# Kernel tuning notes

Measured on AMD Instinct MI355X. Metric: run time of the kernel, lower is better.

Reference implementation:

```python
import jax, jax.numpy as jnp
import numpy as np
import math

N = 50000      # nodes
E = 800000     # edges (avg degree 16)
T = 4          # time steps
F = 64         # feature dim (in = hidden = out)
MAX_LEN = 200  # positional encoding table length
EPS = 1e-5     # BatchNorm eps


def _make_pe(time_dim, max_len):
    pe = np.zeros((max_len, time_dim), dtype=np.float32)
    position = np.arange(max_len, dtype=np.float32)[:, None]
    div_term = np.exp(np.arange(0, time_dim, 2, dtype=np.float32) * (-math.log(10000.0) / time_dim))
    pe[:, 0::2] = np.sin(position * div_term)
    pe[:, 1::2] = np.cos(position * div_term)
    return jnp.asarray(pe)


def setup_inputs() -> dict:
    key = jax.random.key(0)
    ks = jax.random.split(key, 10)
    xav = math.sqrt(2.0 / (F + F))  # xavier_normal_ std for square linear
    return {
        "node_features": jax.random.normal(ks[0], (N, T, F), dtype=jnp.float32),
        "edges_weight": jax.random.uniform(ks[1], (T, E), dtype=jnp.float32),
        "identities": jax.random.randint(ks[2], (T,), 0, MAX_LEN),
        "edge_src": jax.random.randint(ks[3], (E,), 0, N),
        "edge_dst": jax.random.randint(ks[4], (E,), 0, N),
        "pe": _make_pe(F, MAX_LEN),
        "W0": jax.random.normal(ks[5], (F, F), dtype=jnp.float32) * xav,
        "W1": jax.random.normal(ks[6], (F, F), dtype=jnp.float32) * xav,
        "g0": jnp.ones((F,), jnp.float32),
        "b0": jnp.zeros((F,), jnp.float32),
        "g1": jnp.ones((F,), jnp.float32),
        "b1": jnp.zeros((F,), jnp.float32),
    }


def _gcn_layer(h, ew, edge_src, edge_dst, W):
    # gather-mul-scatter: msg_e = h[src_e] * w_e ; agg_v = sum_{e: dst=v} msg_e
    msg = h[edge_src] * ew                                   # (E, T, F)
    agg = jax.ops.segment_sum(msg, edge_dst, num_segments=N)  # (N, T, F)
    readout = agg.mean(axis=0)                                # dgl.mean_nodes (single graph) -> (T, F)
    return agg @ W, readout @ W


def _batchnorm(x, gamma, beta):
    # training-mode batch stats over all non-channel dims
    mean = x.mean(axis=(0, 1))
    var = x.var(axis=(0, 1))
    return (x - mean) * jax.lax.rsqrt(var + EPS) * gamma + beta


def reference(node_features, edges_weight, identities, edge_src, edge_dst,
              pe, W0, W1, g0, b0, g1, b1):
    # positional encoding added per time step
    h = node_features + pe[identities]          # (N, T, F)
    ew = edges_weight.T[:, :, None]             # (E, T, 1)
    # layer 0: gcn -> dropout(eval=identity) -> BN -> ReLU
    h, readout = _gcn_layer(h, ew, edge_src, edge_dst, W0)
    h = jax.nn.relu(_batchnorm(h, g0, b0))
    # layer 1 (output layer)
    h, readout = _gcn_layer(h, ew, edge_src, edge_dst, W1)
    h = jax.nn.relu(_batchnorm(h, g1, b1))
    return h, readout
```

## Files before the change

### kernel.cpp

```cpp
#include <hip/hip_runtime.h>

#define TF 256

typedef __attribute__((ext_vector_type(8))) short short8;
typedef __attribute__((ext_vector_type(4))) float f32x4;
typedef __attribute__((ext_vector_type(4))) unsigned int uint4v;
typedef __attribute__((ext_vector_type(2))) unsigned int uint2v;

__device__ inline unsigned short f2bf(float x) {
  unsigned u = __float_as_uint(x);
  u += 0x7fffu + ((u >> 16) & 1u);
  return (unsigned short)(u >> 16);
}
__device__ inline unsigned pack2(unsigned short lo, unsigned short hi) {
  return (unsigned)lo | ((unsigned)hi << 16);
}
__device__ inline float bflo(unsigned u) { return __uint_as_float(u << 16); }
__device__ inline float bfhi(unsigned u) { return __uint_as_float(u & 0xffff0000u); }

__global__ void prep_hist_kernel(const float* __restrict__ x, const float* __restrict__ pe,
                                 const int* __restrict__ ids, uint2v* __restrict__ h0, int n4,
                                 const int* __restrict__ dst, int* __restrict__ indeg, int E) {
  const int gid = blockIdx.x * blockDim.x + threadIdx.x;
  const int stride = gridDim.x * blockDim.x;
  for (int i = gid; i < n4; i += stride) {
    int e0 = (i << 2) & (TF - 1);
    int t = e0 >> 6;
    int f4 = e0 & 63;
    f32x4 v = __builtin_nontemporal_load(&reinterpret_cast<const f32x4*>(x)[i]);
    const f32x4 p = *reinterpret_cast<const f32x4*>(&pe[ids[t] * 64 + f4]);
    uint2v o;
    o.x = pack2(f2bf(v.x + p.x), f2bf(v.y + p.y));
    o.y = pack2(f2bf(v.z + p.z), f2bf(v.w + p.w));
    h0[i] = o;
  }
  for (int e = gid; e < E; e += stride) {
    atomicAdd(&indeg[__builtin_nontemporal_load(&dst[e])], 1);
  }
}

__global__ __launch_bounds__(1024) void scan_part1(const int* __restrict__ indeg,
                                                   int* __restrict__ partials, int n) {
  __shared__ int wsum[16];
  const int tid = threadIdx.x;
  const int lane = tid & 63;
  const int wid = tid >> 6;
  int i = blockIdx.x * 1024 + tid;
  int s = (i < n) ? indeg[i] : 0;
  #pragma unroll
  for (int o = 1; o < 64; o <<= 1) s += __shfl_xor(s, o, 64);
  if (lane == 0) wsum[wid] = s;
  __syncthreads();
  if (tid == 0) {
    int acc = 0;
    #pragma unroll
    for (int w = 0; w < 16; ++w) acc += wsum[w];
    partials[blockIdx.x] = acc;
  }
}

__global__ __launch_bounds__(512) void scan2_wfrag_kernel(
    const int* __restrict__ partials, int* __restrict__ base, int* __restrict__ offsets,
    int nb, int n, const float* __restrict__ W0, const float* __restrict__ W1,
    short* __restrict__ wf0, short* __restrict__ wf1) {
  const int tid = threadIdx.x;
  if (tid < 64) {
    int v = (tid < nb) ? partials[tid] : 0;
    int s = v;
    #pragma unroll
    for (int o = 1; o < 64; o <<= 1) {
      int t = __shfl_up(s, o, 64);
      if (tid >= o) s += t;
    }
    if (tid < nb) base[tid] = s - v;
    if (tid == nb - 1) offsets[n] = s;
  }
  const int frag = tid >> 6, lane = tid & 63;
  const int c = frag >> 1, h = frag & 1;
  const int col = (c << 4) + (lane & 15);
  const int k0 = h * 32 + ((lane >> 4) << 3);
  short* o0 = wf0 + frag * 512 + lane * 8;
  short* o1 = wf1 + frag * 512 + lane * 8;
  #pragma unroll
  for (int i = 0; i < 8; ++i) {
    o0[i] = (short)f2bf(W0[(k0 + i) * 64 + col]);
    o1[i] = (short)f2bf(W1[(k0 + i) * 64 + col]);
  }
}

__global__ __launch_bounds__(1024) void scan_part3(const int* __restrict__ indeg,
                                                   const int* __restrict__ base,
                                                   int* __restrict__ offsets, int n) {
  __shared__ int wsum[16];
  const int tid = threadIdx.x;
  const int lane = tid & 63;
  const int wid = tid >> 6;
  int i = blockIdx.x * 1024 + tid;
  int v = (i < n) ? indeg[i] : 0;
  int s = v;
  #pragma unroll
  for (int o = 1; o < 64; o <<= 1) {
    int t = __shfl_up(s, o, 64);
    if (lane >= o) s += t;
  }
  if (lane == 63) wsum[wid] = s;
  __syncthreads();
  if (tid == 0) {
    int acc = 0;
    #pragma unroll
    for (int w = 0; w < 16; ++w) { int t = wsum[w]; wsum[w] = acc; acc += t; }
  }
  __syncthreads();
  int excl = s - v + wsum[wid] + base[blockIdx.x];
  if (i < n) offsets[i] = excl;
}

__global__ __launch_bounds__(256) void binscatter_kernel(
    const int* __restrict__ src, const int* __restrict__ dst,
    const float* __restrict__ ew, int* __restrict__ gbin_cursor,
    uint4v* __restrict__ tmp, int E, int nbins) {
  __shared__ int hist[256];
  __shared__ int hist2[256];
  __shared__ int basearr[256];
  const int tid = threadIdx.x;
  hist[tid] = 0;
  hist2[tid] = 0;
  __syncthreads();
  const int epb = (E + gridDim.x - 1) / gridDim.x;
  const int beg = blockIdx.x * epb;
  const int end = min(beg + epb, E);
  for (int e = beg + tid; e < end; e += 256)
    atomicAdd(&hist[__builtin_nontemporal_load(&dst[e]) >> 8], 1);
  __syncthreads();
  if (tid < nbins && hist[tid] > 0)
    basearr[tid] = atomicAdd(&gbin_cursor[tid], hist[tid]);
  __syncthreads();
  for (int e = beg + tid; e < end; e += 256) {
    const int d = dst[e];
    const int bin = d >> 8;
    const int idx = atomicAdd(&hist2[bin], 1);
    uint4v ent;
    ent.x = (unsigned)(src[e] << 9);
    ent.y = pack2(f2bf(ew[e]), f2bf(ew[(size_t)E + e]));
    ent.z = pack2(f2bf(ew[2 * (size_t)E + e]), f2bf(ew[3 * (size_t)E + e]));
    ent.w = (unsigned)d;
    const int pos = basearr[bin] + idx;
    if (pos < 8192)
      __builtin_nontemporal_store(ent, &tmp[((size_t)bin << 13) + pos]);
  }
}

__global__ __launch_bounds__(256) void csr_build_kernel(
    const uint4v* __restrict__ tmp, const int* __restrict__ gbin_cursor,
    const int* __restrict__ offsets, uint4v* __restrict__ csr_ent, int n) {
  __shared__ int cur[256];
  const int bin = blockIdx.x;
  const int tid = threadIdx.x;
  const int node = (bin << 8) + tid;
  cur[tid] = (node < n) ? offsets[node] : 0;
  __syncthreads();
  int cnt = gbin_cursor[bin];
  if (cnt > 8192) cnt = 8192;
  const uint4v* bt = tmp + ((size_t)bin << 13);
  for (int i = tid; i < cnt; i += 256) {
    uint4v ent = __builtin_nontemporal_load(&bt[i]);
    const int local = (int)(ent.w & 255u);
    const int pos = atomicAdd(&cur[local], 1);
    ent.w = 0u;
    __builtin_nontemporal_store(ent, &csr_ent[pos]);
  }
}

template <int LAYER>
__global__ __launch_bounds__(256, 6) void fused_agg_mm_kernel(
    const char* __restrict__ h_base, const int* __restrict__ offsets,
    const uint4v* __restrict__ csr_ent, const short* __restrict__ wf,
    const float* __restrict__ red, const float* __restrict__ g,
    const float* __restrict__ b, float inv_count,
    unsigned short* __restrict__ y_bf, float* __restrict__ part, int n_groups) {
  __shared__ unsigned short tile[2][16][72];
  __shared__ float s_sc[64], s_sh[64];
  const int tid = threadIdx.x;
  const int lane = tid & 63;
  const int wid = tid >> 6;
  if (LAYER == 1) {
    if (tid < 64) {
      float sum = red[tid] + red[64 + tid] + red[128 + tid] + red[192 + tid];
      float mean = sum * inv_count;
      float var = red[256 + tid] * inv_count - mean * mean;
      float sc = g[tid] * rsqrtf(var + 1e-5f);
      s_sc[tid] = sc;
      s_sh[tid] = fmaf(-mean, sc, b[tid]);
    }
    __syncthreads();
  }
  const short8 bf0 = *reinterpret_cast<const short8*>(wf + (wid * 2 + 0) * 512 + lane * 8);
  const short8 bf1 = *reinterpret_cast<const short8*>(wf + (wid * 2 + 1) * 512 + lane * 8);

  const int p = lane >> 5;
  const unsigned q = lane & 31;
  const unsigned qb = q << 4;
  const int tw = q >> 3;

  float scv[8], shv[8];
  if (LAYER == 1) {
    const int f0 = (q & 7) << 3;
    #pragma unroll
    for (int j = 0; j < 8; ++j) { scv[j] = s_sc[f0 + j]; shv[j] = s_sh[f0 + j]; }
  }

  f32x4 csum = (f32x4){0.f, 0.f, 0.f, 0.f};
  float ssq = 0.f;
  int buf = 0;

  for (int grp = blockIdx.x; grp < n_groups; grp += gridDim.x) {
    const int v = grp * 4 + wid;
    float acc[8];
    #pragma unroll
    for (int j = 0; j < 8; ++j) acc[j] = 0.f;

    auto wext = [&](uint4v ent) -> float {
      unsigned word = (tw & 2) ? ent.z : ent.y;
      return (tw & 1) ? bfhi(word) : bflo(word);
    };
    auto body = [&](uint4v u, float w) {
      float x[8] = {bflo(u.x), bfhi(u.x), bflo(u.y), bfhi(u.y),
                    bflo(u.z), bfhi(u.z), bflo(u.w), bfhi(u.w)};
      #pragma unroll
      for (int j = 0; j < 8; ++j) {
        float t = x[j];
        if (LAYER == 1) t = fmaxf(0.f, fmaf(t, scv[j], shv[j]));
        acc[j] = fmaf(w, t, acc[j]);
      }
    };

    const int beg = offsets[v];
    const int end = offsets[v + 1];
    int i = beg;
    for (; i + 8 <= end; i += 8) {
      uint4v ent[4];
      #pragma unroll
      for (int c = 0; c < 4; ++c) ent[c] = csr_ent[i + 2 * c + p];
      uint4v row[4];
      #pragma unroll
      for (int c = 0; c < 4; ++c)
        row[c] = *reinterpret_cast<const uint4v*>(h_base + (ent[c].x + qb));
      #pragma unroll
      for (int c = 0; c < 4; ++c) body(row[c], wext(ent[c]));
    }
    for (; i + 2 <= end; i += 2) {
      const uint4v ent = csr_ent[i + p];
      const uint4v row = *reinterpret_cast<const uint4v*>(h_base + (ent.x + qb));
      body(row, wext(ent));
    }
    if (i < end) {
      const uint4v ent = csr_ent[i];
      const uint4v row = *reinterpret_cast<const uint4v*>(h_base + (ent.x + qb));
      body(row, p == 0 ? wext(ent) : 0.f);
    }

    #pragma unroll
    for (int j = 0; j < 8; ++j) acc[j] += __shfl_xor(acc[j], 32, 64);
    if (lane < 32) {
      uint4v o;
      o.x = pack2(f2bf(acc[0]), f2bf(acc[1]));
      o.y = pack2(f2bf(acc[2]), f2bf(acc[3]));
      o.z = pack2(f2bf(acc[4]), f2bf(acc[5]));
      o.w = pack2(f2bf(acc[6]), f2bf(acc[7]));
      *reinterpret_cast<uint4v*>(&tile[buf][wid * 4 + (q >> 3)][(q & 7) * 8]) = o;
    }
    __syncthreads();

    const int r = lane & 15;
    const int k0 = (lane >> 4) << 3;
    const short8 a0 = *reinterpret_cast<const short8*>(&tile[buf][r][k0]);
    const short8 a1 = *reinterpret_cast<const short8*>(&tile[buf][r][k0 + 32]);
    f32x4 dacc = (f32x4){0.f, 0.f, 0.f, 0.f};
    dacc = __builtin_amdgcn_mfma_f32_16x16x32_bf16(a0, bf0, dacc, 0, 0, 0);
    dacc = __builtin_amdgcn_mfma_f32_16x16x32_bf16(a1, bf1, dacc, 0, 0, 0);
    const int gbase = grp * 16 + ((lane >> 4) << 2);
    const int col = (wid << 4) + (lane & 15);
    #pragma unroll
    for (int i2 = 0; i2 < 4; ++i2) {
      const float val = dacc[i2];
      y_bf[(size_t)(gbase + i2) * 64 + col] = f2bf(val);
      csum[i2] += val;
      ssq += val * val;
    }
    buf ^= 1;
  }

  #pragma unroll
  for (int i2 = 0; i2 < 4; ++i2) {
    float vv = csum[i2];
    vv += __shfl_xor(vv, 16, 64);
    vv += __shfl_xor(vv, 32, 64);
    csum[i2] = vv;
  }
  float qq = ssq;
  qq += __shfl_xor(qq, 16, 64);
  qq += __shfl_xor(qq, 32, 64);
  if (lane < 16) {
    #pragma unroll
    for (int i2 = 0; i2 < 4; ++i2)
      part[(size_t)blockIdx.x * 320 + i2 * 64 + (wid << 4) + lane] = csum[i2];
    part[(size_t)blockIdx.x * 320 + 256 + (wid << 4) + lane] = qq;
  }
}

__global__ __launch_bounds__(1024) void reduce_part_kernel(const float* __restrict__ part,
                                                           float* __restrict__ red, int nblk) {
  __shared__ float lds[1024];
  const int tid = threadIdx.x;
  const int col = blockIdx.x * 16 + (tid & 15);
  const int r = tid >> 4;
  float s = 0.f;
  for (int bk = r; bk < nblk; bk += 64) s += part[(size_t)bk * 320 + col];
  lds[tid] = s;
  __syncthreads();
  #pragma unroll
  for (int off = 512; off >= 16; off >>= 1) {
    if (tid < off) lds[tid] += lds[tid + off];
    __syncthreads();
  }
  if (tid < 16) red[col] = lds[tid];
}

__global__ __launch_bounds__(256) void bn_relu_out_kernel(
    const uint4v* __restrict__ yb, const float* __restrict__ red,
    const float* __restrict__ g, const float* __restrict__ b, float inv_count,
    float* __restrict__ out_readout, float invN, f32x4* __restrict__ out, int n8) {
  __shared__ float s_sc[64], s_sh[64];
  const int tid = threadIdx.x;
  if (tid < 64) {
    float sum = red[tid] + red[64 + tid] + red[128 + tid] + red[192 + tid];
    float mean = sum * inv_count;
    float var = red[256 + tid] * inv_count - mean * mean;
    float sc = g[tid] * rsqrtf(var + 1e-5f);
    s_sc[tid] = sc;
    s_sh[tid] = fmaf(-mean, sc, b[tid]);
  }
  __syncthreads();
  if (blockIdx.x == 0) out_readout[tid] = red[tid] * invN;
  const int i = blockIdx.x * 256 + tid;
  if (i >= n8) return;
  const int f0 = (i & 7) << 3;
  uint4v u = __builtin_nontemporal_load(&yb[i]);
  float x[8] = {bflo(u.x), bfhi(u.x), bflo(u.y), bfhi(u.y),
                bflo(u.z), bfhi(u.z), bflo(u.w), bfhi(u.w)};
  f32x4 o0, o1;
  o0.x = fmaxf(0.f, fmaf(x[0], s_sc[f0 + 0], s_sh[f0 + 0]));
  o0.y = fmaxf(0.f, fmaf(x[1], s_sc[f0 + 1], s_sh[f0 + 1]));
  o0.z = fmaxf(0.f, fmaf(x[2], s_sc[f0 + 2], s_sh[f0 + 2]));
  o0.w = fmaxf(0.f, fmaf(x[3], s_sc[f0 + 3], s_sh[f0 + 3]));
  o1.x = fmaxf(0.f, fmaf(x[4], s_sc[f0 + 4], s_sh[f0 + 4]));
  o1.y = fmaxf(0.f, fmaf(x[5], s_sc[f0 + 5], s_sh[f0 + 5]));
  o1.z = fmaxf(0.f, fmaf(x[6], s_sc[f0 + 6], s_sh[f0 + 6]));
  o1.w = fmaxf(0.f, fmaf(x[7], s_sc[f0 + 7], s_sh[f0 + 7]));
  __builtin_nontemporal_store(o0, &out[i * 2 + 0]);
  __builtin_nontemporal_store(o1, &out[i * 2 + 1]);
}

extern "C" void kernel_launch(void* const* d_in, const int* in_sizes, int n_in,
                              void* d_out, int out_size, void* d_ws, size_t ws_size,
                              hipStream_t stream) {
  const float* node_features = (const float*)d_in[0];
  const float* edges_weight  = (const float*)d_in[1];
  const int*   identities    = (const int*)d_in[2];
  const int*   edge_src      = (const int*)d_in[3];
  const int*   edge_dst      = (const int*)d_in[4];
  const float* pe            = (const float*)d_in[5];
  const float* W0            = (const float*)d_in[6];
  const float* W1            = (const float*)d_in[7];
  const float* g0            = (const float*)d_in[8];
  const float* b0            = (const float*)d_in[9];
  const float* g1            = (const float*)d_in[10];
  const float* b1            = (const float*)d_in[11];

  const int T = in_sizes[2];
  const int E = in_sizes[3];
  const int F = in_sizes[8];
  const int N = in_sizes[0] / (T * F);
  const int R = N * T;
  const int nbins = (N + 255) >> 8;

  float* out = (float*)d_out;
  float* out_h = out;
  float* out_readout = out + (size_t)N * T * F;

  char* ws = (char*)d_ws;
  size_t off = 0;
  auto alloc = [&](size_t bytes) -> void* {
    off = (off + 255) & ~(size_t)255;
    void* p = ws + off;
    off += bytes;
    return p;
  };
  int* zeros = (int*)alloc(((size_t)N + 256) * sizeof(int));
  int* indeg = zeros;
  int* gbin_cursor = zeros + N;
  int*    partials = (int*)alloc(64 * sizeof(int));
  int*    base_    = (int*)alloc(64 * sizeof(int));
  int*    offsets  = (int*)alloc(((size_t)N + 1) * sizeof(int));
  uint4v* csr_ent  = (uint4v*)alloc(((size_t)E + 16) * 16);
  uint4v* tmp      = (uint4v*)alloc(((size_t)nbins << 13) * 16);
  unsigned short* h0b  = (unsigned short*)alloc((size_t)N * TF * 2);
  unsigned short* y0b  = (unsigned short*)alloc((size_t)N * TF * 2);
  short* wf0 = (short*)alloc(8 * 512 * sizeof(short));
  short* wf1 = (short*)alloc(8 * 512 * sizeof(short));
  const int FB = 1536;
  float* mm_part = (float*)alloc((size_t)FB * 320 * sizeof(float));
  float* red     = (float*)alloc(320 * sizeof(float));
  (void)ws_size;

  const int nb = (N + 1023) / 1024;
  const float invR = 1.0f / (float)R;
  const int n_groups = N / 4;

  (void)hipMemsetAsync(zeros, 0, ((size_t)N + 256) * sizeof(int), stream);
  hipLaunchKernelGGL(prep_hist_kernel, dim3(2048), dim3(256), 0, stream,
                     node_features, pe, identities, (uint2v*)h0b, (N * TF) / 4,
                     edge_dst, indeg, E);
  hipLaunchKernelGGL(binscatter_kernel, dim3(256), dim3(256), 0, stream,
                     edge_src, edge_dst, edges_weight, gbin_cursor, tmp, E, nbins);
  hipLaunchKernelGGL(scan_part1, dim3(nb), dim3(1024), 0, stream, indeg, partials, N);
  hipLaunchKernelGGL(scan2_wfrag_kernel, dim3(1), dim3(512), 0, stream,
                     partials, base_, offsets, nb, N, W0, W1, wf0, wf1);
  hipLaunchKernelGGL(scan_part3, dim3(nb), dim3(1024), 0, stream, indeg, base_, offsets, N);
  hipLaunchKernelGGL(csr_build_kernel, dim3(nbins), dim3(256), 0, stream,
                     tmp, gbin_cursor, offsets, csr_ent, N);

  hipLaunchKernelGGL((fused_agg_mm_kernel<0>), dim3(FB), dim3(256), 0, stream,
                     (const char*)h0b, offsets, csr_ent, wf0,
                     nullptr, nullptr, nullptr, 0.f, y0b, mm_part, n_groups);
  hipLaunchKernelGGL(reduce_part_kernel, dim3(20), dim3(1024), 0, stream, mm_part, red, FB);

  hipLaunchKernelGGL((fused_agg_mm_kernel<1>), dim3(FB), dim3(256), 0, stream,
                     (const char*)y0b, offsets, csr_ent, wf1,
                     red, g0, b0, invR, h0b , mm_part, n_groups);
  hipLaunchKernelGGL(reduce_part_kernel, dim3(20), dim3(1024), 0, stream, mm_part, red, FB);

  hipLaunchKernelGGL(bn_relu_out_kernel, dim3((R * 8 + 255) / 256), dim3(256), 0, stream,
                     (const uint4v*)h0b, red, g1, b1, invR,
                     out_readout, 1.0f / (float)N, (f32x4*)out_h, R * 8);
}
```

Baseline: 285.1 us.

## Fold in-degree histogram into binscatter, move prep later, retune grids and occupancy

The per-node in-degree atomic count moves out of the feature-prep kernel into binscatter's first pass, which already reads dst, so dst is read once instead of twice. The prep kernel now runs after CSR build so its bf16 output is fresher in cache for layer 0. Nontemporal hints are dropped on the tmp and CSR stores and loads so those stay cached for the next kernel. Separately, binscatter uses 512 blocks, csr_build uses 512 threads, the fused aggregation kernel targets 8 waves per SIMD, and its grid grows to 2048. The tighter launch bound risks register spills.

```diff
diff --git a/kernel.cpp b/kernel.cpp
--- a/kernel.cpp
+++ b/kernel.cpp
@@ -18,9 +18,8 @@
 __device__ inline float bflo(unsigned u) { return __uint_as_float(u << 16); }
 __device__ inline float bfhi(unsigned u) { return __uint_as_float(u & 0xffff0000u); }
 
-__global__ void prep_hist_kernel(const float* __restrict__ x, const float* __restrict__ pe,
-                                 const int* __restrict__ ids, uint2v* __restrict__ h0, int n4,
-                                 const int* __restrict__ dst, int* __restrict__ indeg, int E) {
+__global__ void prep_kernel(const float* __restrict__ x, const float* __restrict__ pe,
+                            const int* __restrict__ ids, uint2v* __restrict__ h0, int n4) {
   const int gid = blockIdx.x * blockDim.x + threadIdx.x;
   const int stride = gridDim.x * blockDim.x;
   for (int i = gid; i < n4; i += stride) {
@@ -34,9 +33,6 @@
     o.y = pack2(f2bf(v.z + p.z), f2bf(v.w + p.w));
     h0[i] = o;
   }
-  for (int e = gid; e < E; e += stride) {
-    atomicAdd(&indeg[__builtin_nontemporal_load(&dst[e])], 1);
-  }
 }
 
 __global__ __launch_bounds__(1024) void scan_part1(const int* __restrict__ indeg,
@@ -118,7 +114,7 @@
 __global__ __launch_bounds__(256) void binscatter_kernel(
     const int* __restrict__ src, const int* __restrict__ dst,
     const float* __restrict__ ew, int* __restrict__ gbin_cursor,
-    uint4v* __restrict__ tmp, int E, int nbins) {
+    int* __restrict__ indeg, uint4v* __restrict__ tmp, int E, int nbins) {
   __shared__ int hist[256];
   __shared__ int hist2[256];
   __shared__ int basearr[256];
@@ -129,8 +125,11 @@
   const int epb = (E + gridDim.x - 1) / gridDim.x;
   const int beg = blockIdx.x * epb;
   const int end = min(beg + epb, E);
-  for (int e = beg + tid; e < end; e += 256)
-    atomicAdd(&hist[__builtin_nontemporal_load(&dst[e]) >> 8], 1);
+  for (int e = beg + tid; e < end; e += 256) {
+    const int d = __builtin_nontemporal_load(&dst[e]);
+    atomicAdd(&hist[d >> 8], 1);
+    atomicAdd(&indeg[d], 1);
+  }
   __syncthreads();
   if (tid < nbins && hist[tid] > 0)
     basearr[tid] = atomicAdd(&gbin_cursor[tid], hist[tid]);
@@ -146,33 +145,35 @@
     ent.w = (unsigned)d;
     const int pos = basearr[bin] + idx;
     if (pos < 8192)
-      __builtin_nontemporal_store(ent, &tmp[((size_t)bin << 13) + pos]);
-  }
-}
-
-__global__ __launch_bounds__(256) void csr_build_kernel(
+      tmp[((size_t)bin << 13) + pos] = ent;
+  }
+}
+
+__global__ __launch_bounds__(512) void csr_build_kernel(
     const uint4v* __restrict__ tmp, const int* __restrict__ gbin_cursor,
     const int* __restrict__ offsets, uint4v* __restrict__ csr_ent, int n) {
   __shared__ int cur[256];
   const int bin = blockIdx.x;
   const int tid = threadIdx.x;
-  const int node = (bin << 8) + tid;
-  cur[tid] = (node < n) ? offsets[node] : 0;
+  if (tid < 256) {
+    const int node = (bin << 8) + tid;
+    cur[tid] = (node < n) ? offsets[node] : 0;
+  }
   __syncthreads();
   int cnt = gbin_cursor[bin];
   if (cnt > 8192) cnt = 8192;
   const uint4v* bt = tmp + ((size_t)bin << 13);
-  for (int i = tid; i < cnt; i += 256) {
-    uint4v ent = __builtin_nontemporal_load(&bt[i]);
+  for (int i = tid; i < cnt; i += 512) {
+    uint4v ent = bt[i];
     const int local = (int)(ent.w & 255u);
     const int pos = atomicAdd(&cur[local], 1);
     ent.w = 0u;
-    __builtin_nontemporal_store(ent, &csr_ent[pos]);
+    csr_ent[pos] = ent;
   }
 }
 
 template <int LAYER>
-__global__ __launch_bounds__(256, 6) void fused_agg_mm_kernel(
+__global__ __launch_bounds__(256, 8) void fused_agg_mm_kernel(
     const char* __restrict__ h_base, const int* __restrict__ offsets,
     const uint4v* __restrict__ csr_ent, const short* __restrict__ wf,
     const float* __restrict__ red, const float* __restrict__ g,
@@ -408,7 +409,7 @@
   unsigned short* y0b  = (unsigned short*)alloc((size_t)N * TF * 2);
   short* wf0 = (short*)alloc(8 * 512 * sizeof(short));
   short* wf1 = (short*)alloc(8 * 512 * sizeof(short));
-  const int FB = 1536;
+  const int FB = 2048;
   float* mm_part = (float*)alloc((size_t)FB * 320 * sizeof(float));
   float* red     = (float*)alloc(320 * sizeof(float));
   (void)ws_size;
@@ -418,17 +419,16 @@
   const int n_groups = N / 4;
 
   (void)hipMemsetAsync(zeros, 0, ((size_t)N + 256) * sizeof(int), stream);
-  hipLaunchKernelGGL(prep_hist_kernel, dim3(2048), dim3(256), 0, stream,
-                     node_features, pe, identities, (uint2v*)h0b, (N * TF) / 4,
-                     edge_dst, indeg, E);
-  hipLaunchKernelGGL(binscatter_kernel, dim3(256), dim3(256), 0, stream,
-                     edge_src, edge_dst, edges_weight, gbin_cursor, tmp, E, nbins);
+  hipLaunchKernelGGL(binscatter_kernel, dim3(512), dim3(256), 0, stream,
+                     edge_src, edge_dst, edges_weight, gbin_cursor, indeg, tmp, E, nbins);
   hipLaunchKernelGGL(scan_part1, dim3(nb), dim3(1024), 0, stream, indeg, partials, N);
   hipLaunchKernelGGL(scan2_wfrag_kernel, dim3(1), dim3(512), 0, stream,
                      partials, base_, offsets, nb, N, W0, W1, wf0, wf1);
   hipLaunchKernelGGL(scan_part3, dim3(nb), dim3(1024), 0, stream, indeg, base_, offsets, N);
-  hipLaunchKernelGGL(csr_build_kernel, dim3(nbins), dim3(256), 0, stream,
+  hipLaunchKernelGGL(csr_build_kernel, dim3(nbins), dim3(512), 0, stream,
                      tmp, gbin_cursor, offsets, csr_ent, N);
+  hipLaunchKernelGGL(prep_kernel, dim3(2048), dim3(256), 0, stream,
+                     node_features, pe, identities, (uint2v*)h0b, (N * TF) / 4);
 
   hipLaunchKernelGGL((fused_agg_mm_kernel<0>), dim3(FB), dim3(256), 0, stream,
                      (const char*)h0b, offsets, csr_ent, wf0,
```

After: 315.1 us. +10.5%, slower.
